# Kernel tuning notes

Hardware: AMD Instinct MI355X
Metric: run time of the kernel (lower is better)

Reference implementation:

```python
import jax, jax.numpy as jnp
import numpy as np

N = 50000
E = 800000
IN_D, HID_D, EMB_D, K = 128, 128, 64, 16
ALPHA = 1.0
NEG_SLOPE = 0.2


def _l2norm(x, eps=1e-12):
    n = jnp.sqrt(jnp.sum(x * x, axis=1, keepdims=True))
    return x / jnp.maximum(n, eps)


def _gat(x, src, dst, W, a_src, a_dst, b, n_nodes):
    # PyG GATConv, heads=1: h = xW; e_ij = leakyrelu(a_src.h_j + a_dst.h_i)
    h = x @ W                                   # [N, D]
    al_s = h @ a_src                            # [N]
    al_d = h @ a_dst                            # [N]
    logits = jax.nn.leaky_relu(al_s[src] + al_d[dst], NEG_SLOPE)  # [E']
    m = jax.ops.segment_max(logits, dst, num_segments=n_nodes)
    ex = jnp.exp(logits - m[dst])
    denom = jax.ops.segment_sum(ex, dst, num_segments=n_nodes)
    alpha = ex / denom[dst]                     # softmax over incoming edges
    out = jax.ops.segment_sum(h[src] * alpha[:, None], dst, num_segments=n_nodes)
    return out + b


def _cluster_prob(z, cluster):
    z2 = jnp.sum(z * z, axis=1, keepdims=True)          # [N,1]
    c2 = jnp.sum(cluster * cluster, axis=1)[None, :]    # [1,K]
    dist = z2 + c2 - 2.0 * (z @ cluster.T)              # [N,K]
    q = 1.0 / (1.0 + dist / ALPHA)
    q = (q + 1e-07) ** ((ALPHA + 1.0) / 2.0)
    return q / jnp.sum(q, axis=1, keepdims=True)


def setup_inputs() -> dict:
    key = jax.random.key(0)
    ks = jax.random.split(key, 20)
    d = {}
    d['x'] = jax.random.normal(ks[0], (N, IN_D), dtype=jnp.float32)
    d['edge_index'] = jax.random.randint(ks[1], (2, E), 0, N, dtype=jnp.int32)
    dims = [(IN_D, HID_D), (HID_D, EMB_D), (EMB_D, HID_D), (HID_D, IN_D)]
    for i, (di, do) in enumerate(dims):
        s = 1.0 / np.sqrt(di)
        d[f'W{i+1}'] = jax.random.normal(ks[2 + 4 * i], (di, do), dtype=jnp.float32) * s
        d[f'a{i+1}s'] = jax.random.normal(ks[3 + 4 * i], (do,), dtype=jnp.float32) * 0.1
        d[f'a{i+1}d'] = jax.random.normal(ks[4 + 4 * i], (do,), dtype=jnp.float32) * 0.1
        d[f'b{i+1}'] = jnp.zeros((do,), dtype=jnp.float32)
    d['cluster'] = jax.random.normal(ks[18], (K, EMB_D), dtype=jnp.float32) * 0.1
    return d


def reference(x, edge_index, W1, a1s, a1d, b1, W2, a2s, a2d, b2,
              W3, a3s, a3d, b3, W4, a4s, a4d, b4, cluster):
    # add self loops (PyG GATConv default)
    loop = jnp.arange(N, dtype=edge_index.dtype)
    src = jnp.concatenate([edge_index[0], loop])
    dst = jnp.concatenate([edge_index[1], loop])

    xn = _l2norm(x)
    h1 = jax.nn.relu(_gat(xn, src, dst, W1, a1s, a1d, b1, N))
    z = _gat(h1, src, dst, W2, a2s, a2d, b2, N)
    z = _l2norm(z)
    d1 = jax.nn.relu(_gat(z, src, dst, W3, a3s, a3d, b3, N))
    x_hat = _gat(d1, src, dst, W4, a4s, a4d, b4, N)
    q = _cluster_prob(z, cluster)
    return (z, x_hat, q)
```

## Files before the change

kernel.cpp:

```cpp
#include <hip/hip_runtime.h>

#define NN 50000
#define NE 800000
#define NBK 196
#define BCAP 8192
#define GEMM_NB 782

typedef unsigned int uint;
typedef unsigned short ushort;
typedef __attribute__((ext_vector_type(8))) short short8v;
typedef __attribute__((ext_vector_type(4))) float float4v;

static __device__ __forceinline__ float waveReduceSum(float v) {
#pragma unroll
  for (int o = 32; o > 0; o >>= 1) v += __shfl_xor(v, o);
  return v;
}
static __device__ __forceinline__ float waveReduceMax(float v) {
#pragma unroll
  for (int o = 32; o > 0; o >>= 1) v = fmaxf(v, __shfl_xor(v, o));
  return v;
}
static __device__ __forceinline__ float bf_lo(uint u) { return __uint_as_float(u << 16); }
static __device__ __forceinline__ float bf_hi(uint u) { return __uint_as_float(u & 0xffff0000u); }
static __device__ __forceinline__ uint f2bf(float f) {
  uint u = __float_as_uint(f);
  return (u + 0x7fffu + ((u >> 16) & 1u)) >> 16;
}
static __device__ __forceinline__ int waveInclScan(int v, int lane) {
#pragma unroll
  for (int o = 1; o < 64; o <<= 1) {
    int u = __shfl_up(v, o);
    if (lane >= o) v += u;
  }
  return v;
}
static __device__ __forceinline__ void split8(const float* f, short8v& hi, short8v& lo) {
#pragma unroll
  for (int j = 0; j < 8; ++j) {
    uint h = f2bf(f[j]);
    hi[j] = (short)h;
    float hf = __uint_as_float(h << 16);
    lo[j] = (short)f2bf(f[j] - hf);
  }
}

__global__ void k_zero(int* bcnt) {
  if (threadIdx.x < NBK) bcnt[threadIdx.x] = 0;
}
__global__ __launch_bounds__(256) void k_bucket(
    const int* __restrict__ esrc, const int* __restrict__ edst,
    uint* __restrict__ ebuf, int* __restrict__ bcnt) {
  __shared__ int hist[NBK];
  __shared__ int gbase[NBK];
  int tid = threadIdx.x;
  for (int i = tid; i < NBK; i += 256) hist[i] = 0;
  __syncthreads();
  const int ET = NE + NN;
  int base = blockIdx.x * 4096;
  int myb[16];
  uint mypk[16];
#pragma unroll
  for (int j = 0; j < 16; ++j) {
    int e = base + j * 256 + tid;
    int s, d;
    if (e < NE) { s = esrc[e]; d = edst[e]; }
    else if (e < ET) { s = e - NE; d = s; }
    else { myb[j] = -1; continue; }
    int b = d >> 8;
    myb[j] = b;
    mypk[j] = (uint)s | ((uint)(d & 255) << 16);
    atomicAdd(&hist[b], 1);
  }
  __syncthreads();
  for (int i = tid; i < NBK; i += 256) {
    int h = hist[i];
    gbase[i] = h > 0 ? atomicAdd(&bcnt[i], h) : 0;
    hist[i] = 0;
  }
  __syncthreads();
#pragma unroll
  for (int j = 0; j < 16; ++j) {
    int b = myb[j];
    if (b < 0) continue;
    int r = atomicAdd(&hist[b], 1);
    int pos = gbase[b] + r;
    if (pos < BCAP) ebuf[(size_t)b * BCAP + pos] = mypk[j];
  }
}
__global__ __launch_bounds__(256) void k_csr(
    const uint* __restrict__ ebuf, const int* __restrict__ bcnt,
    int* __restrict__ indptr, int* __restrict__ srcs) {
  __shared__ int h[256];
  __shared__ int cur[256];
  __shared__ int wsm[4];
  __shared__ int bbs;
  int tid = threadIdx.x, b = blockIdx.x;
  int lane = tid & 63, wv = tid >> 6;
  int v = (tid < NBK) ? bcnt[tid] : 0;
  int inc = waveInclScan(v, lane);
  if (lane == 63) wsm[wv] = inc;
  __syncthreads();
  int woff = 0;
  for (int k = 0; k < wv; ++k) woff += wsm[k];
  if (tid == b) bbs = inc - v + woff;
  h[tid] = 0;
  __syncthreads();
  int bbase = bbs;
  int cnt = bcnt[b];
  const uint* eb = ebuf + (size_t)b * BCAP;
  for (int i = tid; i < cnt; i += 256) atomicAdd(&h[eb[i] >> 16], 1);
  __syncthreads();
  int hv = h[tid];
  int inc2 = waveInclScan(hv, lane);
  if (lane == 63) wsm[wv] = inc2;
  __syncthreads();
  int woff2 = 0;
  for (int k = 0; k < wv; ++k) woff2 += wsm[k];
  int nodeExcl = inc2 - hv + woff2;
  int node = b * 256 + tid;
  if (node < NN) indptr[node] = bbase + nodeExcl;
  if (node == NN - 1) indptr[NN] = bbase + nodeExcl + hv;
  cur[tid] = nodeExcl;
  __syncthreads();
  for (int i = tid; i < cnt; i += 256) {
    uint pk = eb[i];
    int r = atomicAdd(&cur[pk >> 16], 1);
    srcs[bbase + r] = (int)(pk & 0xffffu);
  }
}

template <int K, int DO, bool NORM>
__global__ __launch_bounds__(256) void k_gemm_mfma(
    const float* __restrict__ X, const float* __restrict__ W,
    const float* __restrict__ avs, const float* __restrict__ avd,
    ushort* __restrict__ H, float* __restrict__ als, float* __restrict__ ald, int n) {
  constexpr int KS = K / 32, CT = DO / 16;
  __shared__ ushort sWhi[K * DO];
  __shared__ ushort sWlo[K * DO];
  __shared__ float sas[DO], sad[DO];
  int tid = threadIdx.x;
  for (int i = tid; i < DO; i += 256) { sas[i] = avs[i]; sad[i] = avd[i]; }
  for (int i = tid; i < K * DO; i += 256) {
    int k = i / DO, col = i & (DO - 1);
    float w = W[i];
    uint h = f2bf(w);
    float hf = __uint_as_float(h << 16);
    uint lo = f2bf(w - hf);
    int fo = (((k >> 5) * CT + (col >> 4)) * 64 + ((col & 15) | (((k >> 3) & 3) << 4))) * 8 + (k & 7);
    sWhi[fo] = (ushort)h;
    sWlo[fo] = (ushort)lo;
  }
  __syncthreads();
  int lane = tid & 63, wv = tid >> 6;
  int r0 = blockIdx.x * 64 + wv * 16;
  if (r0 >= n) return;
  int row = r0 + (lane & 15);
  int sub = lane >> 4;
  const float* xrow = X + (size_t)row * K;
  float xr[KS][8];
#pragma unroll
  for (int s = 0; s < KS; ++s) {
    *(float4*)&xr[s][0] = *(const float4*)(xrow + s * 32 + sub * 8);
    *(float4*)&xr[s][4] = *(const float4*)(xrow + s * 32 + sub * 8 + 4);
  }
  if (NORM) {
    float ss = 0.f;
#pragma unroll
    for (int s = 0; s < KS; ++s)
#pragma unroll
      for (int j = 0; j < 8; ++j) ss += xr[s][j] * xr[s][j];
    ss += __shfl_xor(ss, 16);
    ss += __shfl_xor(ss, 32);
    float sc = 1.0f / fmaxf(sqrtf(ss), 1e-12f);
#pragma unroll
    for (int s = 0; s < KS; ++s)
#pragma unroll
      for (int j = 0; j < 8; ++j) xr[s][j] *= sc;
  }
  float4v acc[CT];
#pragma unroll
  for (int c = 0; c < CT; ++c) acc[c] = (float4v){0.f, 0.f, 0.f, 0.f};
#pragma unroll
  for (int s = 0; s < KS; ++s) {
    short8v ahi, alo;
    split8(xr[s], ahi, alo);
#pragma unroll
    for (int c = 0; c < CT; ++c) {
      short8v bhi = *(const short8v*)&sWhi[(s * CT + c) * 512 + lane * 8];
      short8v blo = *(const short8v*)&sWlo[(s * CT + c) * 512 + lane * 8];
      acc[c] = __builtin_amdgcn_mfma_f32_16x16x32_bf16(ahi, bhi, acc[c], 0, 0, 0);
      acc[c] = __builtin_amdgcn_mfma_f32_16x16x32_bf16(ahi, blo, acc[c], 0, 0, 0);
      acc[c] = __builtin_amdgcn_mfma_f32_16x16x32_bf16(alo, bhi, acc[c], 0, 0, 0);
    }
  }
  int rbase = r0 + (sub << 2);
  float alsp[4] = {0.f, 0.f, 0.f, 0.f};
  float aldp[4] = {0.f, 0.f, 0.f, 0.f};
#pragma unroll
  for (int c = 0; c < CT; ++c) {
    int col = (c << 4) + (lane & 15);
    float as_ = sas[col], ad_ = sad[col];
#pragma unroll
    for (int j = 0; j < 4; ++j) {
      float v = acc[c][j];
      alsp[j] += v * as_;
      aldp[j] += v * ad_;
      uint bv = f2bf(v);
      uint nb = __shfl_xor(bv, 1);
      if (!(lane & 1)) {
        *(uint*)&H[(size_t)(rbase + j) * DO + col] = bv | (nb << 16);
      }
    }
  }
#pragma unroll
  for (int j = 0; j < 4; ++j) {
    float vs = alsp[j], vd = aldp[j];
#pragma unroll
    for (int o = 1; o < 16; o <<= 1) { vs += __shfl_xor(vs, o); vd += __shfl_xor(vd, o); }
    if ((lane & 15) == 0) { als[rbase + j] = vs; ald[rbase + j] = vd; }
  }
}

template <int D, int MODE>
__global__ __launch_bounds__(256) void k_attn_aggr(
    const int* __restrict__ indptr, const int* __restrict__ srcs,
    const float* __restrict__ als, const float* __restrict__ ald,
    const ushort* __restrict__ H, const float* __restrict__ bias,
    float* __restrict__ out, int n) {
  constexpr int CAP = 256;
  __shared__ float slg[4][CAP];
  __shared__ int ssrc[4][CAP];
  int w = (blockIdx.x * blockDim.x + threadIdx.x) >> 6;
  int l = threadIdx.x & 63;
  int wv = threadIdx.x >> 6;
  if (w >= n) return;
  int s0 = indptr[w], s1 = indptr[w + 1];
  int deg = s1 - s0;
  float ad = ald[w];
  float inv;
  float ax = 0.f, ay = 0.f, az = 0.f, aw = 0.f;
  const uint2* Hr = (const uint2*)H;
  if (deg <= CAP) {
    float mx = -1e30f;
    for (int t = l; t < deg; t += 64) {
      int s = srcs[s0 + t];
      float v = als[s] + ad;
      v = v >= 0.f ? v : 0.2f * v;
      ssrc[wv][t] = s;
      slg[wv][t] = v;
      mx = fmaxf(mx, v);
    }
    mx = waveReduceMax(mx);
    float sum = 0.f;
    for (int t = l; t < deg; t += 64) {
      float e = __expf(slg[wv][t] - mx);
      slg[wv][t] = e;
      sum += e;
    }
    sum = waveReduceSum(sum);
    inv = 1.0f / sum;
    if (D == 128) {
      int g = l >> 5, j = l & 31;
      int i = 0;
      for (; i + 16 <= deg; i += 16) {
        float p[8]; int e[8]; uint2 u[8];
#pragma unroll
        for (int r = 0; r < 8; ++r) { int idx = i + 2 * r + g; p[r] = slg[wv][idx]; e[r] = ssrc[wv][idx]; }
#pragma unroll
        for (int r = 0; r < 8; ++r) u[r] = Hr[(size_t)e[r] * 32 + j];
#pragma unroll
        for (int r = 0; r < 8; ++r) {
          ax += p[r] * bf_lo(u[r].x); ay += p[r] * bf_hi(u[r].x);
          az += p[r] * bf_lo(u[r].y); aw += p[r] * bf_hi(u[r].y);
        }
      }
      for (; i + 8 <= deg; i += 8) {
        float p[4]; int e[4]; uint2 u[4];
#pragma unroll
        for (int r = 0; r < 4; ++r) { int idx = i + 2 * r + g; p[r] = slg[wv][idx]; e[r] = ssrc[wv][idx]; }
#pragma unroll
        for (int r = 0; r < 4; ++r) u[r] = Hr[(size_t)e[r] * 32 + j];
#pragma unroll
        for (int r = 0; r < 4; ++r) {
          ax += p[r] * bf_lo(u[r].x); ay += p[r] * bf_hi(u[r].x);
          az += p[r] * bf_lo(u[r].y); aw += p[r] * bf_hi(u[r].y);
        }
      }
      for (; i < deg; i += 2) {
        int idx = i + g;
        if (idx < deg) {
          float p = slg[wv][idx];
          uint2 u = Hr[(size_t)ssrc[wv][idx] * 32 + j];
          ax += p * bf_lo(u.x); ay += p * bf_hi(u.x);
          az += p * bf_lo(u.y); aw += p * bf_hi(u.y);
        }
      }
    } else {
      int g = l >> 4, j = l & 15;
      int i = 0;
      for (; i + 32 <= deg; i += 32) {
        float p[8]; int e[8]; uint2 u[8];
#pragma unroll
        for (int r = 0; r < 8; ++r) { int idx = i + 4 * r + g; p[r] = slg[wv][idx]; e[r] = ssrc[wv][idx]; }
#pragma unroll
        for (int r = 0; r < 8; ++r) u[r] = Hr[(size_t)e[r] * 16 + j];
#pragma unroll
        for (int r = 0; r < 8; ++r) {
          ax += p[r] * bf_lo(u[r].x); ay += p[r] * bf_hi(u[r].x);
          az += p[r] * bf_lo(u[r].y); aw += p[r] * bf_hi(u[r].y);
        }
      }
      for (; i + 16 <= deg; i += 16) {
        float p[4]; int e[4]; uint2 u[4];
#pragma unroll
        for (int r = 0; r < 4; ++r) { int idx = i + 4 * r + g; p[r] = slg[wv][idx]; e[r] = ssrc[wv][idx]; }
#pragma unroll
        for (int r = 0; r < 4; ++r) u[r] = Hr[(size_t)e[r] * 16 + j];
#pragma unroll
        for (int r = 0; r < 4; ++r) {
          ax += p[r] * bf_lo(u[r].x); ay += p[r] * bf_hi(u[r].x);
          az += p[r] * bf_lo(u[r].y); aw += p[r] * bf_hi(u[r].y);
        }
      }
      for (; i < deg; i += 4) {
        int idx = i + g;
        if (idx < deg) {
          float p = slg[wv][idx];
          uint2 u = Hr[(size_t)ssrc[wv][idx] * 16 + j];
          ax += p * bf_lo(u.x); ay += p * bf_hi(u.x);
          az += p * bf_lo(u.y); aw += p * bf_hi(u.y);
        }
      }
    }
  } else {
    float mx = -1e30f;
    for (int t = l; t < deg; t += 64) {
      int s = srcs[s0 + t];
      float v = als[s] + ad;
      v = v >= 0.f ? v : 0.2f * v;
      mx = fmaxf(mx, v);
    }
    mx = waveReduceMax(mx);
    float sum = 0.f;
    for (int t = l; t < deg; t += 64) {
      int s = srcs[s0 + t];
      float v = als[s] + ad;
      v = v >= 0.f ? v : 0.2f * v;
      sum += __expf(v - mx);
    }
    sum = waveReduceSum(sum);
    inv = 1.0f / sum;
    for (int base = 0; base < deg; base += 64) {
      int t = base + l;
      if (t < deg) {
        int s = srcs[s0 + t];
        float v = als[s] + ad;
        v = v >= 0.f ? v : 0.2f * v;
        ssrc[wv][l] = s;
        slg[wv][l] = __expf(v - mx);
      }
      __builtin_amdgcn_wave_barrier();
      int m = min(64, deg - base);
      if (D == 128) {
        int g = l >> 5, j = l & 31;
        for (int i2 = g; i2 < m; i2 += 2) {
          float p = slg[wv][i2];
          uint2 u = Hr[(size_t)ssrc[wv][i2] * 32 + j];
          ax += p * bf_lo(u.x); ay += p * bf_hi(u.x);
          az += p * bf_lo(u.y); aw += p * bf_hi(u.y);
        }
      } else {
        int g = l >> 4, j = l & 15;
        for (int i2 = g; i2 < m; i2 += 4) {
          float p = slg[wv][i2];
          uint2 u = Hr[(size_t)ssrc[wv][i2] * 16 + j];
          ax += p * bf_lo(u.x); ay += p * bf_hi(u.x);
          az += p * bf_lo(u.y); aw += p * bf_hi(u.y);
        }
      }
      __builtin_amdgcn_wave_barrier();
    }
  }
  if (D == 128) {
    ax += __shfl_xor(ax, 32); ay += __shfl_xor(ay, 32);
    az += __shfl_xor(az, 32); aw += __shfl_xor(aw, 32);
    if (l < 32) {
      float4 bv = ((const float4*)bias)[l];
      float v0 = ax * inv + bv.x, v1 = ay * inv + bv.y;
      float v2 = az * inv + bv.z, v3 = aw * inv + bv.w;
      if (MODE == 1) {
        v0 = fmaxf(v0, 0.f); v1 = fmaxf(v1, 0.f);
        v2 = fmaxf(v2, 0.f); v3 = fmaxf(v3, 0.f);
      }
      ((float4*)(out + (size_t)w * 128))[l] = make_float4(v0, v1, v2, v3);
    }
  } else {
    ax += __shfl_xor(ax, 16); ay += __shfl_xor(ay, 16);
    az += __shfl_xor(az, 16); aw += __shfl_xor(aw, 16);
    ax += __shfl_xor(ax, 32); ay += __shfl_xor(ay, 32);
    az += __shfl_xor(az, 32); aw += __shfl_xor(aw, 32);
    int j = l & 15;
    float4 bv = ((const float4*)bias)[j];
    float v0 = ax * inv + bv.x, v1 = ay * inv + bv.y;
    float v2 = az * inv + bv.z, v3 = aw * inv + bv.w;
    if (MODE == 2) {
      float ss = v0 * v0 + v1 * v1 + v2 * v2 + v3 * v3;
      ss += __shfl_xor(ss, 1); ss += __shfl_xor(ss, 2);
      ss += __shfl_xor(ss, 4); ss += __shfl_xor(ss, 8);
      float sc = 1.0f / fmaxf(sqrtf(ss), 1e-12f);
      v0 *= sc; v1 *= sc; v2 *= sc; v3 *= sc;
    }
    if (l < 16) ((float4*)(out + (size_t)w * 64))[j] = make_float4(v0, v1, v2, v3);
  }
}

__global__ void k_q(const float* __restrict__ z, const float* __restrict__ cl,
                    float* __restrict__ q, int n) {
  int w = (blockIdx.x * blockDim.x + threadIdx.x) >> 6;
  int l = threadIdx.x & 63;
  if (w >= n) return;
  int k = l >> 2, p = l & 3;
  const float* zr = z + (size_t)w * 64 + p * 16;
  const float* cr = cl + k * 64 + p * 16;
  float s = 0.f;
#pragma unroll
  for (int d = 0; d < 16; ++d) {
    float df = zr[d] - cr[d];
    s += df * df;
  }
  s += __shfl_xor(s, 1);
  s += __shfl_xor(s, 2);
  float qv = 1.0f / (1.0f + s) + 1e-7f;
  float t = qv;
  t += __shfl_xor(t, 4);
  t += __shfl_xor(t, 8);
  t += __shfl_xor(t, 16);
  t += __shfl_xor(t, 32);
  float rs = t;
  if (p == 0) q[(size_t)w * 16 + k] = qv / rs;
}

extern "C" void kernel_launch(void* const* d_in, const int* in_sizes, int n_in,
                              void* d_out, int out_size, void* d_ws, size_t ws_size,
                              hipStream_t stream) {
  const float* x = (const float*)d_in[0];
  const int* ei = (const int*)d_in[1];
  const float* W1 = (const float*)d_in[2];
  const float* a1s = (const float*)d_in[3];
  const float* a1d = (const float*)d_in[4];
  const float* b1 = (const float*)d_in[5];
  const float* W2 = (const float*)d_in[6];
  const float* a2s = (const float*)d_in[7];
  const float* a2d = (const float*)d_in[8];
  const float* b2 = (const float*)d_in[9];
  const float* W3 = (const float*)d_in[10];
  const float* a3s = (const float*)d_in[11];
  const float* a3d = (const float*)d_in[12];
  const float* b3 = (const float*)d_in[13];
  const float* W4 = (const float*)d_in[14];
  const float* a4s = (const float*)d_in[15];
  const float* a4d = (const float*)d_in[16];
  const float* b4 = (const float*)d_in[17];
  const float* cluster = (const float*)d_in[18];

  float* out = (float*)d_out;
  float* z = out;
  float* xhat = out + (size_t)NN * 64;
  float* qout = xhat + (size_t)NN * 128;

  const int ET = NE + NN;
  float* wsf = (float*)d_ws;
  float* X = wsf;          wsf += (size_t)NN * 128;
  ushort* H = (ushort*)wsf; wsf += (size_t)NN * 64;
  float* als = wsf;        wsf += NN;
  float* ald = wsf;        wsf += NN;
  int* indptr = (int*)wsf; wsf += NN + 1;
  int* srcs = (int*)wsf;   wsf += ET;
  uint* ebuf = (uint*)wsf; wsf += (size_t)NBK * BCAP;
  int* bcnt = (int*)wsf;   wsf += NBK;

  const int* esrc = ei;
  const int* edst = ei + NE;

  const int TB = 256;
  const int gW = (NN + 3) / 4;
  const int gB = (ET + 4095) / 4096;

  k_zero<<<1, 256, 0, stream>>>(bcnt);
  k_bucket<<<gB, 256, 0, stream>>>(esrc, edst, ebuf, bcnt);
  k_csr<<<NBK, 256, 0, stream>>>(ebuf, bcnt, indptr, srcs);

  k_gemm_mfma<128, 128, true><<<GEMM_NB, 256, 0, stream>>>(x, W1, a1s, a1d, H, als, ald, NN);
  k_attn_aggr<128, 1><<<gW, TB, 0, stream>>>(indptr, srcs, als, ald, H, b1, X, NN);

  k_gemm_mfma<128, 64, false><<<GEMM_NB, 256, 0, stream>>>(X, W2, a2s, a2d, H, als, ald, NN);
  k_attn_aggr<64, 2><<<gW, TB, 0, stream>>>(indptr, srcs, als, ald, H, b2, z, NN);

  k_gemm_mfma<64, 128, false><<<GEMM_NB, 256, 0, stream>>>(z, W3, a3s, a3d, H, als, ald, NN);
  k_attn_aggr<128, 1><<<gW, TB, 0, stream>>>(indptr, srcs, als, ald, H, b3, X, NN);

  k_gemm_mfma<128, 128, false><<<GEMM_NB, 256, 0, stream>>>(X, W4, a4s, a4d, H, als, ald, NN);
  k_attn_aggr<128, 0><<<gW, TB, 0, stream>>>(indptr, srcs, als, ald, H, b4, xhat, NN);

  k_q<<<gW, TB, 0, stream>>>(z, cluster, qout, NN);
}
```

Measured before the change: 293.2 us.

## Precompute split bf16 weights once, persist GEMM blocks, fuse cluster-prob into layer-2 aggregation

Result: faster. 254.1 us (-13.3%).

```diff
diff --git a/kernel.cpp b/kernel.cpp
--- a/kernel.cpp
+++ b/kernel.cpp
@@ -4,7 +4,8 @@
 #define NE 800000
 #define NBK 196
 #define BCAP 8192
-#define GEMM_NB 782
+#define GEMM_GRID 391
+#define WTOT 49152
 
 typedef unsigned int uint;
 typedef unsigned short ushort;
@@ -130,95 +131,119 @@
   }
 }
 
+__global__ void k_wprep(const float* __restrict__ W1, const float* __restrict__ W2,
+                        const float* __restrict__ W3, const float* __restrict__ W4,
+                        ushort* __restrict__ hi, ushort* __restrict__ lo) {
+  int i = blockIdx.x * 256 + threadIdx.x;
+  if (i >= WTOT) return;
+  const float* W; int DO, base;
+  if (i < 16384)      { W = W1; DO = 128; base = 0; }
+  else if (i < 24576) { W = W2; DO = 64;  base = 16384; }
+  else if (i < 32768) { W = W3; DO = 128; base = 24576; }
+  else                { W = W4; DO = 128; base = 32768; }
+  int idx = i - base;
+  int k = idx / DO, col = idx % DO;
+  float w = W[idx];
+  uint h = f2bf(w);
+  float hf = __uint_as_float(h << 16);
+  uint l2 = f2bf(w - hf);
+  int CT = DO >> 4;
+  int fo = base + (((k >> 5) * CT + (col >> 4)) * 64 + ((col & 15) | (((k >> 3) & 3) << 4))) * 8 + (k & 7);
+  hi[fo] = (ushort)h;
+  lo[fo] = (ushort)l2;
+}
+
 template <int K, int DO, bool NORM>
 __global__ __launch_bounds__(256) void k_gemm_mfma(
-    const float* __restrict__ X, const float* __restrict__ W,
+    const float* __restrict__ X, const ushort* __restrict__ Whi,
+    const ushort* __restrict__ Wlo,
     const float* __restrict__ avs, const float* __restrict__ avd,
     ushort* __restrict__ H, float* __restrict__ als, float* __restrict__ ald, int n) {
   constexpr int KS = K / 32, CT = DO / 16;
+  constexpr int W4N = K * DO / 8;
   __shared__ ushort sWhi[K * DO];
   __shared__ ushort sWlo[K * DO];
   __shared__ float sas[DO], sad[DO];
   int tid = threadIdx.x;
   for (int i = tid; i < DO; i += 256) { sas[i] = avs[i]; sad[i] = avd[i]; }
-  for (int i = tid; i < K * DO; i += 256) {
-    int k = i / DO, col = i & (DO - 1);
-    float w = W[i];
-    uint h = f2bf(w);
-    float hf = __uint_as_float(h << 16);
-    uint lo = f2bf(w - hf);
-    int fo = (((k >> 5) * CT + (col >> 4)) * 64 + ((col & 15) | (((k >> 3) & 3) << 4))) * 8 + (k & 7);
-    sWhi[fo] = (ushort)h;
-    sWlo[fo] = (ushort)lo;
+  {
+    const uint4* ghi = (const uint4*)Whi;
+    const uint4* glo = (const uint4*)Wlo;
+    uint4* shi = (uint4*)sWhi;
+    uint4* slo = (uint4*)sWlo;
+    for (int i = tid; i < W4N; i += 256) { shi[i] = ghi[i]; slo[i] = glo[i]; }
   }
   __syncthreads();
   int lane = tid & 63, wv = tid >> 6;
-  int r0 = blockIdx.x * 64 + wv * 16;
-  if (r0 >= n) return;
-  int row = r0 + (lane & 15);
-  int sub = lane >> 4;
-  const float* xrow = X + (size_t)row * K;
-  float xr[KS][8];
-#pragma unroll
-  for (int s = 0; s < KS; ++s) {
-    *(float4*)&xr[s][0] = *(const float4*)(xrow + s * 32 + sub * 8);
-    *(float4*)&xr[s][4] = *(const float4*)(xrow + s * 32 + sub * 8 + 4);
-  }
-  if (NORM) {
-    float ss = 0.f;
-#pragma unroll
-    for (int s = 0; s < KS; ++s)
-#pragma unroll
-      for (int j = 0; j < 8; ++j) ss += xr[s][j] * xr[s][j];
-    ss += __shfl_xor(ss, 16);
-    ss += __shfl_xor(ss, 32);
-    float sc = 1.0f / fmaxf(sqrtf(ss), 1e-12f);
-#pragma unroll
-    for (int s = 0; s < KS; ++s)
-#pragma unroll
-      for (int j = 0; j < 8; ++j) xr[s][j] *= sc;
-  }
-  float4v acc[CT];
-#pragma unroll
-  for (int c = 0; c < CT; ++c) acc[c] = (float4v){0.f, 0.f, 0.f, 0.f};
-#pragma unroll
-  for (int s = 0; s < KS; ++s) {
-    short8v ahi, alo;
-    split8(xr[s], ahi, alo);
+  int ntiles = (n + 63) >> 6;
+  for (int tile = blockIdx.x; tile < ntiles; tile += gridDim.x) {
+    int r0 = tile * 64 + wv * 16;
+    if (r0 >= n) continue;
+    int row = r0 + (lane & 15);
+    int sub = lane >> 4;
+    const float* xrow = X + (size_t)row * K;
+    float xr[KS][8];
+#pragma unroll
+    for (int s = 0; s < KS; ++s) {
+      *(float4*)&xr[s][0] = *(const float4*)(xrow + s * 32 + sub * 8);
+      *(float4*)&xr[s][4] = *(const float4*)(xrow + s * 32 + sub * 8 + 4);
+    }
+    if (NORM) {
+      float ss = 0.f;
+#pragma unroll
+      for (int s = 0; s < KS; ++s)
+#pragma unroll
+        for (int j = 0; j < 8; ++j) ss += xr[s][j] * xr[s][j];
+      ss += __shfl_xor(ss, 16);
+      ss += __shfl_xor(ss, 32);
+      float sc = 1.0f / fmaxf(sqrtf(ss), 1e-12f);
+#pragma unroll
+      for (int s = 0; s < KS; ++s)
+#pragma unroll
+        for (int j = 0; j < 8; ++j) xr[s][j] *= sc;
+    }
+    float4v acc[CT];
+#pragma unroll
+    for (int c = 0; c < CT; ++c) acc[c] = (float4v){0.f, 0.f, 0.f, 0.f};
+#pragma unroll
+    for (int s = 0; s < KS; ++s) {
+      short8v ahi, alo;
+      split8(xr[s], ahi, alo);
+#pragma unroll
+      for (int c = 0; c < CT; ++c) {
+        short8v bhi = *(const short8v*)&sWhi[(s * CT + c) * 512 + lane * 8];
+        short8v blo = *(const short8v*)&sWlo[(s * CT + c) * 512 + lane * 8];
+        acc[c] = __builtin_amdgcn_mfma_f32_16x16x32_bf16(ahi, bhi, acc[c], 0, 0, 0);
+        acc[c] = __builtin_amdgcn_mfma_f32_16x16x32_bf16(ahi, blo, acc[c], 0, 0, 0);
+        acc[c] = __builtin_amdgcn_mfma_f32_16x16x32_bf16(alo, bhi, acc[c], 0, 0, 0);
+      }
+    }
+    int rbase = r0 + (sub << 2);
+    float alsp[4] = {0.f, 0.f, 0.f, 0.f};
+    float aldp[4] = {0.f, 0.f, 0.f, 0.f};
 #pragma unroll
     for (int c = 0; c < CT; ++c) {
-      short8v bhi = *(const short8v*)&sWhi[(s * CT + c) * 512 + lane * 8];
-      short8v blo = *(const short8v*)&sWlo[(s * CT + c) * 512 + lane * 8];
-      acc[c] = __builtin_amdgcn_mfma_f32_16x16x32_bf16(ahi, bhi, acc[c], 0, 0, 0);
-      acc[c] = __builtin_amdgcn_mfma_f32_16x16x32_bf16(ahi, blo, acc[c], 0, 0, 0);
-      acc[c] = __builtin_amdgcn_mfma_f32_16x16x32_bf16(alo, bhi, acc[c], 0, 0, 0);
-    }
-  }
-  int rbase = r0 + (sub << 2);
-  float alsp[4] = {0.f, 0.f, 0.f, 0.f};
-  float aldp[4] = {0.f, 0.f, 0.f, 0.f};
-#pragma unroll
-  for (int c = 0; c < CT; ++c) {
-    int col = (c << 4) + (lane & 15);
-    float as_ = sas[col], ad_ = sad[col];
+      int col = (c << 4) + (lane & 15);
+      float as_ = sas[col], ad_ = sad[col];
+#pragma unroll
+      for (int j = 0; j < 4; ++j) {
+        float v = acc[c][j];
+        alsp[j] += v * as_;
+        aldp[j] += v * ad_;
+        uint bv = f2bf(v);
+        uint nb = __shfl_xor(bv, 1);
+        if (!(lane & 1)) {
+          *(uint*)&H[(size_t)(rbase + j) * DO + col] = bv | (nb << 16);
+        }
+      }
+    }
 #pragma unroll
     for (int j = 0; j < 4; ++j) {
-      float v = acc[c][j];
-      alsp[j] += v * as_;
-      aldp[j] += v * ad_;
-      uint bv = f2bf(v);
-      uint nb = __shfl_xor(bv, 1);
-      if (!(lane & 1)) {
-        *(uint*)&H[(size_t)(rbase + j) * DO + col] = bv | (nb << 16);
-      }
-    }
-  }
-#pragma unroll
-  for (int j = 0; j < 4; ++j) {
-    float vs = alsp[j], vd = aldp[j];
-#pragma unroll
-    for (int o = 1; o < 16; o <<= 1) { vs += __shfl_xor(vs, o); vd += __shfl_xor(vd, o); }
-    if ((lane & 15) == 0) { als[rbase + j] = vs; ald[rbase + j] = vd; }
+      float vs = alsp[j], vd = aldp[j];
+#pragma unroll
+      for (int o = 1; o < 16; o <<= 1) { vs += __shfl_xor(vs, o); vd += __shfl_xor(vd, o); }
+      if ((lane & 15) == 0) { als[rbase + j] = vs; ald[rbase + j] = vd; }
+    }
   }
 }
 
@@ -227,13 +252,20 @@
     const int* __restrict__ indptr, const int* __restrict__ srcs,
     const float* __restrict__ als, const float* __restrict__ ald,
     const ushort* __restrict__ H, const float* __restrict__ bias,
-    float* __restrict__ out, int n) {
+    float* __restrict__ out, const float* __restrict__ cluster,
+    float* __restrict__ qout, int n) {
   constexpr int CAP = 256;
   __shared__ float slg[4][CAP];
   __shared__ int ssrc[4][CAP];
+  __shared__ float scl[MODE == 2 ? 1024 : 4];
+  __shared__ float sz[4][MODE == 2 ? 64 : 4];
   int w = (blockIdx.x * blockDim.x + threadIdx.x) >> 6;
   int l = threadIdx.x & 63;
   int wv = threadIdx.x >> 6;
+  if (MODE == 2) {
+    for (int i = threadIdx.x; i < 1024; i += 256) scl[i] = cluster[i];
+    __syncthreads();
+  }
   if (w >= n) return;
   int s0 = indptr[w], s1 = indptr[w + 1];
   int deg = s1 - s0;
@@ -412,33 +444,29 @@
       v0 *= sc; v1 *= sc; v2 *= sc; v3 *= sc;
     }
     if (l < 16) ((float4*)(out + (size_t)w * 64))[j] = make_float4(v0, v1, v2, v3);
-  }
-}
-
-__global__ void k_q(const float* __restrict__ z, const float* __restrict__ cl,
-                    float* __restrict__ q, int n) {
-  int w = (blockIdx.x * blockDim.x + threadIdx.x) >> 6;
-  int l = threadIdx.x & 63;
-  if (w >= n) return;
-  int k = l >> 2, p = l & 3;
-  const float* zr = z + (size_t)w * 64 + p * 16;
-  const float* cr = cl + k * 64 + p * 16;
-  float s = 0.f;
-#pragma unroll
-  for (int d = 0; d < 16; ++d) {
-    float df = zr[d] - cr[d];
-    s += df * df;
-  }
-  s += __shfl_xor(s, 1);
-  s += __shfl_xor(s, 2);
-  float qv = 1.0f / (1.0f + s) + 1e-7f;
-  float t = qv;
-  t += __shfl_xor(t, 4);
-  t += __shfl_xor(t, 8);
-  t += __shfl_xor(t, 16);
-  t += __shfl_xor(t, 32);
-  float rs = t;
-  if (p == 0) q[(size_t)w * 16 + k] = qv / rs;
+    if (MODE == 2) {
+      if (l < 16) ((float4*)&sz[wv][0])[j] = make_float4(v0, v1, v2, v3);
+      __builtin_amdgcn_wave_barrier();
+      int kk = l >> 2, p = l & 3;
+      const float* zr = &sz[wv][p * 16];
+      const float* cr = &scl[kk * 64 + p * 16];
+      float s = 0.f;
+#pragma unroll
+      for (int d = 0; d < 16; ++d) {
+        float df = zr[d] - cr[d];
+        s += df * df;
+      }
+      s += __shfl_xor(s, 1);
+      s += __shfl_xor(s, 2);
+      float qv = 1.0f / (1.0f + s) + 1e-7f;
+      float t = qv;
+      t += __shfl_xor(t, 4);
+      t += __shfl_xor(t, 8);
+      t += __shfl_xor(t, 16);
+      t += __shfl_xor(t, 32);
+      if (p == 0) qout[(size_t)w * 16 + kk] = qv / t;
+    }
+  }
 }
 
 extern "C" void kernel_launch(void* const* d_in, const int* in_sizes, int n_in,
@@ -479,6 +507,8 @@
   int* srcs = (int*)wsf;   wsf += ET;
   uint* ebuf = (uint*)wsf; wsf += (size_t)NBK * BCAP;
   int* bcnt = (int*)wsf;   wsf += NBK;
+  ushort* wfhi = (ushort*)wsf; wsf += WTOT / 2;
+  ushort* wflo = (ushort*)wsf; wsf += WTOT / 2;
 
   const int* esrc = ei;
   const int* edst = ei + NE;
@@ -488,20 +518,27 @@
   const int gB = (ET + 4095) / 4096;
 
   k_zero<<<1, 256, 0, stream>>>(bcnt);
+  k_wprep<<<(WTOT + 255) / 256, 256, 0, stream>>>(W1, W2, W3, W4, wfhi, wflo);
   k_bucket<<<gB, 256, 0, stream>>>(esrc, edst, ebuf, bcnt);
   k_csr<<<NBK, 256, 0, stream>>>(ebuf, bcnt, indptr, srcs);
 
-  k_gemm_mfma<128, 128, true><<<GEMM_NB, 256, 0, stream>>>(x, W1, a1s, a1d, H, als, ald, NN);
-  k_attn_aggr<128, 1><<<gW, TB, 0, stream>>>(indptr, srcs, als, ald, H, b1, X, NN);
-
-  k_gemm_mfma<128, 64, false><<<GEMM_NB, 256, 0, stream>>>(X, W2, a2s, a2d, H, als, ald, NN);
-  k_attn_aggr<64, 2><<<gW, TB, 0, stream>>>(indptr, srcs, als, ald, H, b2, z, NN);
-
-  k_gemm_mfma<64, 128, false><<<GEMM_NB, 256, 0, stream>>>(z, W3, a3s, a3d, H, als, ald, NN);
-  k_attn_aggr<128, 1><<<gW, TB, 0, stream>>>(indptr, srcs, als, ald, H, b3, X, NN);
-
-  k_gemm_mfma<128, 128, false><<<GEMM_NB, 256, 0, stream>>>(X, W4, a4s, a4d, H, als, ald, NN);
-  k_attn_aggr<128, 0><<<gW, TB, 0, stream>>>(indptr, srcs, als, ald, H, b4, xhat, NN);
-
-  k_q<<<gW, TB, 0, stream>>>(z, cluster, qout, NN);
-}
+  k_gemm_mfma<128, 128, true><<<GEMM_GRID, 256, 0, stream>>>(
+      x, wfhi, wflo, a1s, a1d, H, als, ald, NN);
+  k_attn_aggr<128, 1><<<gW, TB, 0, stream>>>(indptr, srcs, als, ald, H, b1, X,
+                                             nullptr, nullptr, NN);
+
+  k_gemm_mfma<128, 64, false><<<GEMM_GRID, 256, 0, stream>>>(
+      X, wfhi + 16384, wflo + 16384, a2s, a2d, H, als, ald, NN);
+  k_attn_aggr<64, 2><<<gW, TB, 0, stream>>>(indptr, srcs, als, ald, H, b2, z,
+                                            cluster, qout, NN);
+
+  k_gemm_mfma<64, 128, false><<<GEMM_GRID, 256, 0, stream>>>(
+      z, wfhi + 24576, wflo + 24576, a3s, a3d, H, als, ald, NN);
+  k_attn_aggr<128, 1><<<gW, TB, 0, stream>>>(indptr, srcs, als, ald, H, b3, X,
+                                             nullptr, nullptr, NN);
+
+  k_gemm_mfma<128, 128, false><<<GEMM_GRID, 256, 0, stream>>>(
+      X, wfhi + 32768, wflo + 32768, a4s, a4d, H, als, ald, NN);
+  k_attn_aggr<128, 0><<<gW, TB, 0, stream>>>(indptr, srcs, als, ald, H, b4, xhat,
+                                             nullptr, nullptr, NN);
+}
```
